# Performance work log

Hardware: AMD Instinct MI355X
Metric: run time of the kernel (lower is better)

The kernel has to match this reference:

```python
import jax, jax.numpy as jnp
import numpy as np

B, L = 4, 1024
V, D, H, NL = 32000, 256, 4, 8
S, DC, DI, NTYPES = 16, 4, 512, 5  # d_state, d_conv, d_inner=expand*d_model
NM, NA = 6, 2  # mamba blocks (layers 0,1,2,4,5,6), attention blocks (layers 3,7)


def layernorm(x, g, b):
    m = x.mean(-1, keepdims=True)
    v = x.var(-1, keepdims=True)
    return (x - m) / jnp.sqrt(v + 1e-5) * g + b


def mamba_block(x, g, b, in_w, conv_w, conv_b, xproj_w, dt_w, dt_b, A_log, Dp, out_w):
    res = x
    xn = layernorm(x, g, b)
    xz = xn @ in_w.T                          # [B,L,2*DI]
    xb, z = jnp.split(xz, 2, axis=-1)
    # depthwise causal conv1d (torch pads both sides then truncates to L == left-pad only)
    xc = jnp.transpose(xb, (0, 2, 1))         # [B,DI,L]
    xc = jax.lax.conv_general_dilated(xc, conv_w, (1,), [(DC - 1, 0)], feature_group_count=DI)
    xc = xc + conv_b[None, :, None]
    xb = jax.nn.silu(jnp.transpose(xc, (0, 2, 1)))  # [B,L,DI]
    A = -jnp.exp(A_log)                        # [DI,S]
    Bm, Cm = jnp.split(xb @ xproj_w.T, 2, axis=-1)  # each [B,L,S]
    dt = jax.nn.softplus(xb @ dt_w.T + dt_b)   # [B,L,DI]

    def step(h, inp):
        dt_t, B_t, C_t, x_t = inp              # [B,DI],[B,S],[B,S],[B,DI]
        A_bar = jnp.exp(dt_t[:, :, None] * A)  # [B,DI,S]
        h = A_bar * h + (dt_t * x_t)[:, :, None] * B_t[:, None, :]
        y = (h * C_t[:, None, :]).sum(-1) + Dp * x_t
        return h, y

    h0 = jnp.zeros((x.shape[0], DI, S), x.dtype)
    xs = (jnp.swapaxes(dt, 0, 1), jnp.swapaxes(Bm, 0, 1), jnp.swapaxes(Cm, 0, 1), jnp.swapaxes(xb, 0, 1))
    _, ys = jax.lax.scan(step, h0, xs)         # ys: [L,B,DI]
    y = jnp.swapaxes(ys, 0, 1) * jax.nn.silu(z)
    return y @ out_w.T + res


def attn_block(x, ts, mask, g, b, qkv_w, out_w, decay, ffg, ffb, ff1, ff2):
    Bs, Lq, Dm = x.shape
    dh = Dm // H
    res = x
    xn = layernorm(x, g, b)
    qkv = (xn @ qkv_w.T).reshape(Bs, Lq, 3, H, dh)
    q, k, v = qkv[:, :, 0], qkv[:, :, 1], qkv[:, :, 2]   # [B,L,H,dh]
    attn = jnp.einsum('bqhd,bkhd->bhqk', q, k) * dh ** -0.5
    t_diff = jnp.abs(ts[:, :, None] - ts[:, None, :])[:, None] / 24.0   # [B,1,L,L]
    attn = attn - jax.nn.softplus(decay)[None, :, None, None] * t_diff
    causal = jnp.triu(jnp.ones((Lq, Lq), bool), 1)
    attn = jnp.where(causal[None, None], -jnp.inf, attn)
    attn = jnp.where((mask == 0)[:, None, None, :], -jnp.inf, attn)
    attn = jax.nn.softmax(attn, axis=-1)       # dropout inactive (eval)
    out = jnp.einsum('bhqk,bkhd->bqhd', attn, v).reshape(Bs, Lq, Dm)
    x = res + out @ out_w.T
    xn2 = layernorm(x, ffg, ffb)
    return x + jax.nn.silu(xn2 @ ff1.T) @ ff2.T


def setup_inputs():
    key = jax.random.key(0)
    ks = iter(jax.random.split(key, 64))
    rn = lambda shape, s=0.02: jax.random.normal(next(ks), shape, jnp.float32) * s
    A_init = jnp.log(jnp.tile(jnp.arange(1, S + 1, dtype=jnp.float32)[None, None, :], (NM, DI, 1)))
    return dict(
        token_ids=jax.random.randint(next(ks), (B, L), 0, V, jnp.int32),
        token_types=jax.random.randint(next(ks), (B, L), 0, NTYPES, jnp.int32),
        timestamps=jax.random.uniform(next(ks), (B, L), jnp.float32) * 100.0,
        attention_mask=jnp.ones((B, L), jnp.int32),
        tok_emb=rn((V, D)).at[0].set(0.0),  # padding_idx=0
        type_emb=rn((NTYPES, D)),
        te_freq=rn((D // 2,), 0.01), te_phase=jnp.zeros((D // 2,)),
        te_w=rn((D, D)), te_b=jnp.zeros((D,)),
        m_norm_g=jnp.ones((NM, D)), m_norm_b=jnp.zeros((NM, D)),
        m_in_w=rn((NM, 2 * DI, D)),
        m_conv_w=rn((NM, DI, 1, DC)), m_conv_b=jnp.zeros((NM, DI)),
        m_xproj_w=rn((NM, 2 * S, DI)),
        m_dt_w=rn((NM, DI, DI)), m_dt_b=jnp.zeros((NM, DI)),
        m_Alog=A_init, m_D=jnp.ones((NM, DI)),
        m_out_w=rn((NM, D, DI)),
        a_norm_g=jnp.ones((NA, D)), a_norm_b=jnp.zeros((NA, D)),
        a_qkv_w=rn((NA, 3 * D, D)), a_out_w=rn((NA, D, D)),
        a_decay=jnp.full((NA, H), 0.01, jnp.float32),
        a_ffg=jnp.ones((NA, D)), a_ffb=jnp.zeros((NA, D)),
        a_ff1=rn((NA, 4 * D, D)), a_ff2=rn((NA, D, 4 * D)),
        f_g=jnp.ones((D,)), f_b=jnp.zeros((D,)),
        lm_w=rn((V, D)),
        re_w=rn((1, D)), re_b=jnp.zeros((1,)),
        mo_w=rn((1, D)), mo_b=jnp.zeros((1,)),
    )


def reference(token_ids, token_types, timestamps, attention_mask,
              tok_emb, type_emb, te_freq, te_phase, te_w, te_b,
              m_norm_g, m_norm_b, m_in_w, m_conv_w, m_conv_b, m_xproj_w,
              m_dt_w, m_dt_b, m_Alog, m_D, m_out_w,
              a_norm_g, a_norm_b, a_qkv_w, a_out_w, a_decay, a_ffg, a_ffb, a_ff1, a_ff2,
              f_g, f_b, lm_w, re_w, re_b, mo_w, mo_b):
    t = timestamps[..., None]
    freq = jax.nn.softplus(te_freq)
    enc = jnp.concatenate([jnp.sin(t * freq + te_phase), jnp.cos(t * freq + te_phase)], -1) @ te_w.T + te_b
    x = tok_emb[token_ids] + type_emb[token_types] + enc
    mi = ai = 0
    for i in range(NL):
        if (i + 1) % 4 == 0:
            x = attn_block(x, timestamps, attention_mask,
                           a_norm_g[ai], a_norm_b[ai], a_qkv_w[ai], a_out_w[ai], a_decay[ai],
                           a_ffg[ai], a_ffb[ai], a_ff1[ai], a_ff2[ai])
            ai += 1
        else:
            x = mamba_block(x, m_norm_g[mi], m_norm_b[mi], m_in_w[mi], m_conv_w[mi], m_conv_b[mi],
                            m_xproj_w[mi], m_dt_w[mi], m_dt_b[mi], m_Alog[mi], m_D[mi], m_out_w[mi])
            mi += 1
    x = layernorm(x, f_g, f_b)
    cls = x[:, 0, :]
    lm_logits = x @ lm_w.T
    readm = (cls @ re_w.T + re_b)[:, 0]
    mort = (cls @ mo_w.T + mo_b)[:, 0]
    return lm_logits, readm, mort
```

## Files before the change

### kernel.cpp

```cpp
#include <hip/hip_runtime.h>
#include <hip/hip_bf16.h>
#include <math.h>

#define BB 4
#define LL 1024
#define BL (BB*LL)
#define DD 256
#define VV 32000
#define HH 4
#define DH 64
#define SS 16
#define DCC 4
#define DII 512

typedef float f32x4 __attribute__((ext_vector_type(4)));
typedef short bh8  __attribute__((ext_vector_type(8)));
typedef unsigned short u16;

__device__ __forceinline__ float sp_f(float x) {
    return fmaxf(x, 0.f) + log1pf(expf(-fabsf(x)));
}
__device__ __forceinline__ float silu_f(float x) {
    return x / (1.f + expf(-x));
}
__device__ __forceinline__ short f2bf(float f) {
    __hip_bfloat16 h = __float2bfloat16(f);
    short s; __builtin_memcpy(&s, &h, 2); return s;
}
__device__ __forceinline__ float bf2f(u16 u) {
    unsigned v = ((unsigned)u) << 16;
    float f; __builtin_memcpy(&f, &v, 4); return f;
}

#define WB_TOT 5668864
#define LM_TOT 8192000
__global__ void cvtall_k(const float* __restrict__ te_w, const float* __restrict__ a_qkv,
                         const float* __restrict__ a_out, const float* __restrict__ a_ff1,
                         const float* __restrict__ a_ff2, const float* __restrict__ m_in,
                         const float* __restrict__ m_out, const float* __restrict__ m_dt,
                         const float* __restrict__ m_xp, const float* __restrict__ lm,
                         u16* __restrict__ dst, u16* __restrict__ dlm) {
    long i = ((long)blockIdx.x * 256 + threadIdx.x) * 4;
    const float* src; long off; u16* d; long doff;
    if (i >= WB_TOT) {
        long j = i - WB_TOT;
        if (j >= LM_TOT) return;
        src = lm; off = j; d = dlm; doff = j;
    } else {
        d = dst; doff = i;
        if      (i < 65536)   { src = te_w;  off = i; }
        else if (i < 458752)  { src = a_qkv; off = i - 65536; }
        else if (i < 589824)  { src = a_out; off = i - 458752; }
        else if (i < 1114112) { src = a_ff1; off = i - 589824; }
        else if (i < 1638400) { src = a_ff2; off = i - 1114112; }
        else if (i < 3211264) { src = m_in;  off = i - 1638400; }
        else if (i < 3997696) { src = m_out; off = i - 3211264; }
        else {
            long l = i - 3997696;
            int mi = (int)(l / 278528);
            long r = l - (long)mi * 278528;
            if (r < 262144) { src = m_dt + (long)mi * 262144; off = r; }
            else            { src = m_xp + (long)mi * 16384;  off = r - 262144; }
        }
    }
    float4 v = *(const float4*)(src + off);
    ushort4 u;
    u.x = (u16)f2bf(v.x); u.y = (u16)f2bf(v.y);
    u.z = (u16)f2bf(v.z); u.w = (u16)f2bf(v.w);
    *(ushort4*)(d + doff) = u;
}

__global__ void feat_k(const float* __restrict__ ts, const float* __restrict__ freq,
                       const float* __restrict__ phase, u16* __restrict__ feat) {
    int row = blockIdx.x, t = threadIdx.x;
    float tv = ts[row];
    int d = t & 127;
    float f = sp_f(freq[d]);
    float arg = tv * f + phase[d];
    feat[(size_t)row * DD + t] = (u16)f2bf((t < 128) ? sinf(arg) : cosf(arg));
}

__global__ void ln_k(const float* __restrict__ x, const float* __restrict__ g,
                     const float* __restrict__ bbias, u16* __restrict__ out) {
    __shared__ float red[8];
    int row = blockIdx.x, t = threadIdx.x;
    float v = x[(size_t)row * DD + t];
    float s = v;
    #pragma unroll
    for (int o = 32; o >= 1; o >>= 1) s += __shfl_xor(s, o);
    if ((t & 63) == 0) red[t >> 6] = s;
    __syncthreads();
    float mean = (red[0] + red[1] + red[2] + red[3]) * (1.f / 256.f);
    float d = v - mean;
    float s2 = d * d;
    #pragma unroll
    for (int o = 32; o >= 1; o >>= 1) s2 += __shfl_xor(s2, o);
    if ((t & 63) == 0) red[4 + (t >> 6)] = s2;
    __syncthreads();
    float var = (red[4] + red[5] + red[6] + red[7]) * (1.f / 256.f);
    out[(size_t)row * DD + t] = (u16)f2bf(d * rsqrtf(var + 1e-5f) * g[t] + bbias[t]);
}

template <int ACT, bool BOUT, bool VT>
__global__ __launch_bounds__(256) void lngemm_k(
    const float* __restrict__ X, const float* __restrict__ g, const float* __restrict__ bb,
    const u16* __restrict__ W, void* __restrict__ outv, u16* __restrict__ vt,
    int M, int N) {
    __shared__ __align__(16) char Abf[32768];
    __shared__ __align__(16) char Ws[8192];
    __shared__ float gs[256], bs[256];
    int tid = threadIdx.x;
    int bm = blockIdx.y * 64, bn = blockIdx.x * 64;
    gs[tid] = g[tid]; bs[tid] = bb[tid];

    int row = tid >> 2, part = tid & 3;
    const float* xr = X + (size_t)(bm + row) * 256 + part * 64;
    float4 vv[16];
    float s = 0.f, sq = 0.f;
    #pragma unroll
    for (int i = 0; i < 16; ++i) {
        vv[i] = *(const float4*)(xr + i * 4);
        s  += vv[i].x + vv[i].y + vv[i].z + vv[i].w;
        sq += vv[i].x * vv[i].x + vv[i].y * vv[i].y + vv[i].z * vv[i].z + vv[i].w * vv[i].w;
    }
    s += __shfl_xor(s, 1);  s += __shfl_xor(s, 2);
    sq += __shfl_xor(sq, 1); sq += __shfl_xor(sq, 2);
    float mean = s * (1.f / 256.f);
    float rstd = rsqrtf(sq * (1.f / 256.f) - mean * mean + 1e-5f);
    __syncthreads();
    #pragma unroll
    for (int i8 = 0; i8 < 8; ++i8) {
        bh8 p;
        #pragma unroll
        for (int j = 0; j < 8; ++j) {
            int e = i8 * 8 + j;
            float v = (j & 3) == 0 ? vv[e >> 2].x : (j & 3) == 1 ? vv[e >> 2].y
                    : (j & 3) == 2 ? vv[e >> 2].z : vv[e >> 2].w;
            int c = part * 64 + e;
            p[j] = f2bf((v - mean) * rstd * gs[c] + bs[c]);
        }
        *(bh8*)(Abf + (unsigned)((row * 512 + part * 128 + i8 * 16) ^ ((row & 7) << 4))) = p;
    }
    __syncthreads();

    int lane = tid & 63, wv = tid >> 6;
    int wm = wv >> 1, wn = wv & 1;
    int ro = lane & 15, kg = lane >> 4;
    f32x4 acc[2][2];
    #pragma unroll
    for (int i = 0; i < 2; ++i)
        #pragma unroll
        for (int j = 0; j < 2; ++j) acc[i][j] = (f32x4){0.f, 0.f, 0.f, 0.f};

    const u16* gw = W + (size_t)(bn + row) * 256 + part * 16;
    bool wvalid = (bn + row) < N;
    unsigned swb = (unsigned)(row * 128 + part * 32);
    unsigned sx  = (unsigned)((row & 7) << 4);
    for (int kk = 0; kk < 256; kk += 64) {
        if (kk) __syncthreads();
        bh8 w0 = {}, w1 = {};
        if (wvalid) { w0 = *(const bh8*)(gw + kk); w1 = *(const bh8*)(gw + kk + 8); }
        *(bh8*)(Ws + (swb ^ sx)) = w0;
        *(bh8*)(Ws + ((swb + 16) ^ sx)) = w1;
        __syncthreads();
        #pragma unroll
        for (int ks = 0; ks < 2; ++ks) {
            bh8 af[2], bf_[2];
            #pragma unroll
            for (int m = 0; m < 2; ++m) {
                int r = wm * 32 + m * 16 + ro;
                af[m] = *(const bh8*)(Abf + (unsigned)((r * 512 + kk * 2 + ks * 64 + kg * 16) ^ ((r & 7) << 4)));
            }
            #pragma unroll
            for (int n = 0; n < 2; ++n) {
                int r = wn * 32 + n * 16 + ro;
                bf_[n] = *(const bh8*)(Ws + (unsigned)((r * 128 + ks * 64 + kg * 16) ^ ((r & 7) << 4)));
            }
            #pragma unroll
            for (int m = 0; m < 2; ++m)
                #pragma unroll
                for (int n = 0; n < 2; ++n)
                    acc[m][n] = __builtin_amdgcn_mfma_f32_16x16x32_bf16(af[m], bf_[n], acc[m][n], 0, 0, 0);
        }
    }

    float* outf = (float*)outv;
    u16*   outb = (u16*)outv;
    int cr = (lane >> 4) * 4, cc = lane & 15;
    #pragma unroll
    for (int mf = 0; mf < 2; ++mf) {
        #pragma unroll
        for (int nf = 0; nf < 2; ++nf) {
            int n = bn + wn * 32 + nf * 16 + cc;
            if (n >= N) continue;
            int mbase = bm + wm * 32 + mf * 16 + cr;
            f32x4 a = acc[mf][nf];
            #pragma unroll
            for (int r = 0; r < 4; ++r) {
                float v = a[r];
                if (ACT == 1) v = silu_f(v);
                if (BOUT) outb[(size_t)(mbase + r) * N + n] = (u16)f2bf(v);
                else      outf[(size_t)(mbase + r) * N + n] = v;
            }
            if (VT && n >= 512) {
                int hh = (n - 512) >> 6, dd = (n - 512) & 63;
                int b_ = mbase >> 10, l = mbase & 1023;
                ushort4 uv;
                uv.x = (u16)f2bf(acc[mf][nf][0]); uv.y = (u16)f2bf(acc[mf][nf][1]);
                uv.z = (u16)f2bf(acc[mf][nf][2]); uv.w = (u16)f2bf(acc[mf][nf][3]);
                *(ushort4*)(vt + ((((size_t)b_ * HH + hh) * DH + dd) << 10) + l) = uv;
            }
        }
    }
}

template <int ACT, bool HASB, bool HASR, bool BOUT>
__global__ __launch_bounds__(256) void bgemm_k(
    const u16* __restrict__ A, const u16* __restrict__ W,
    const float* __restrict__ bias, const float* __restrict__ res,
    void* __restrict__ outv, float* __restrict__ out2, int M, int N, int K,
    const int* __restrict__ ids, const int* __restrict__ typ,
    const float* __restrict__ tok, const float* __restrict__ tpe) {
    __shared__ __align__(16) char lds[16384];
    char* As = lds;
    char* Ws = lds + 8192;
    int tid = threadIdx.x;
    int bm = blockIdx.y * 64, bn = blockIdx.x * 64;
    int row = tid >> 2, q = tid & 3;
    int lane = tid & 63, wv = tid >> 6;
    int wm = wv >> 1, wn = wv & 1;
    int ro = lane & 15, kg = lane >> 4;

    f32x4 acc[2][2];
    #pragma unroll
    for (int i = 0; i < 2; ++i)
        #pragma unroll
        for (int j = 0; j < 2; ++j) acc[i][j] = (f32x4){0.f, 0.f, 0.f, 0.f};

    const u16* ga = A + (size_t)(bm + row) * K + q * 16;
    const u16* gw = W + (size_t)(bn + row) * K + q * 16;
    bool wvalid = (bn + row) < N;
    unsigned swb = (unsigned)(row * 128 + q * 32);
    unsigned sx  = (unsigned)((row & 7) << 4);

    for (int kk = 0; kk < K; kk += 64) {
        if (kk) __syncthreads();
        {
            *(bh8*)(As + (swb ^ sx)) = *(const bh8*)(ga);
            *(bh8*)(As + ((swb + 16) ^ sx)) = *(const bh8*)(ga + 8);
            bh8 w0 = {}, w1 = {};
            if (wvalid) { w0 = *(const bh8*)(gw); w1 = *(const bh8*)(gw + 8); }
            *(bh8*)(Ws + (swb ^ sx)) = w0;
            *(bh8*)(Ws + ((swb + 16) ^ sx)) = w1;
        }
        ga += 64; gw += 64;
        __syncthreads();
        #pragma unroll
        for (int ks = 0; ks < 2; ++ks) {
            bh8 af[2], bf_[2];
            #pragma unroll
            for (int m = 0; m < 2; ++m) {
                int r = wm * 32 + m * 16 + ro;
                af[m] = *(const bh8*)(As + (unsigned)((r * 128 + ks * 64 + kg * 16) ^ ((r & 7) << 4)));
            }
            #pragma unroll
            for (int n = 0; n < 2; ++n) {
                int r = wn * 32 + n * 16 + ro;
                bf_[n] = *(const bh8*)(Ws + (unsigned)((r * 128 + ks * 64 + kg * 16) ^ ((r & 7) << 4)));
            }
            #pragma unroll
            for (int m = 0; m < 2; ++m)
                #pragma unroll
                for (int n = 0; n < 2; ++n)
                    acc[m][n] = __builtin_amdgcn_mfma_f32_16x16x32_bf16(af[m], bf_[n], acc[m][n], 0, 0, 0);
        }
    }

    float* outf = (float*)outv;
    u16*   outb = (u16*)outv;
    int cr = (lane >> 4) * 4, cc = lane & 15;
    #pragma unroll
    for (int mf = 0; mf < 2; ++mf) {
        #pragma unroll
        for (int nf = 0; nf < 2; ++nf) {
            int n = bn + wn * 32 + nf * 16 + cc;
            if (n >= N) continue;
            int mbase = bm + wm * 32 + mf * 16 + cr;
            f32x4 a = acc[mf][nf];
            #pragma unroll
            for (int r = 0; r < 4; ++r) {
                float v = a[r];
                int m = mbase + r;
                if (ACT == 3) {
                    if (n < 512) outf[(size_t)m * 512 + n] = sp_f(v + bias[n]);
                    else         out2[(size_t)m * 32 + (n - 512)] = v;
                } else if (ACT == 4) {
                    v += bias[n] + tok[(size_t)ids[m] * DD + n] + tpe[(size_t)typ[m] * DD + n];
                    outf[(size_t)m * N + n] = v;
                } else {
                    if (HASB) v += bias[n];
                    if (ACT == 1) v = silu_f(v);
                    if (HASR) v += res[(size_t)m * N + n];
                    if (BOUT) outb[(size_t)m * N + n] = (u16)f2bf(v);
                    else      outf[(size_t)m * N + n] = v;
                }
            }
        }
    }
}

__global__ __launch_bounds__(256) void mgemmL_k(
    const u16* __restrict__ A, const u16* __restrict__ W,
    float* __restrict__ out, int M, int N, int K) {
    __shared__ __align__(16) char lds[32768];
    char* As = lds;
    char* Ws = lds + 16384;
    int lid = blockIdx.y * 32 + blockIdx.x;
    int xcd = lid & 7, wk = lid >> 3;
    int nt = xcd * 32 + (wk >> 5);
    int mt = wk & 31;
    if (nt * 128 >= N) return;
    int bm = mt * 128, bn = nt * 128;

    int tid = threadIdx.x;
    int row = tid >> 1, half = tid & 1;
    int lane = tid & 63, wv = tid >> 6;
    int wm = wv >> 1, wn = wv & 1;
    int ro = lane & 15, kg = lane >> 4;

    f32x4 acc[4][4];
    #pragma unroll
    for (int i = 0; i < 4; ++i)
        #pragma unroll
        for (int j = 0; j < 4; ++j) acc[i][j] = (f32x4){0.f, 0.f, 0.f, 0.f};

    const u16* ga = A + (size_t)(bm + row) * K + half * 32;
    const u16* gw = W + (size_t)(bn + row) * K + half * 32;
    unsigned swb = (unsigned)(row * 128 + half * 64);
    unsigned sx  = (unsigned)((row & 7) << 4);

    for (int kk = 0; kk < K; kk += 64) {
        if (kk) __syncthreads();
        #pragma unroll
        for (int j = 0; j < 4; ++j) {
            *(bh8*)(As + ((swb + j * 16) ^ sx)) = *(const bh8*)(ga + j * 8);
            *(bh8*)(Ws + ((swb + j * 16) ^ sx)) = *(const bh8*)(gw + j * 8);
        }
        ga += 64; gw += 64;
        __syncthreads();
        #pragma unroll
        for (int ks = 0; ks < 2; ++ks) {
            bh8 af[4], bf_[4];
            #pragma unroll
            for (int m = 0; m < 4; ++m) {
                int r = wm * 64 + m * 16 + ro;
                af[m] = *(const bh8*)(As + (unsigned)((r * 128 + ks * 64 + kg * 16) ^ ((r & 7) << 4)));
            }
            #pragma unroll
            for (int n = 0; n < 4; ++n) {
                int r = wn * 64 + n * 16 + ro;
                bf_[n] = *(const bh8*)(Ws + (unsigned)((r * 128 + ks * 64 + kg * 16) ^ ((r & 7) << 4)));
            }
            #pragma unroll
            for (int m = 0; m < 4; ++m)
                #pragma unroll
                for (int n = 0; n < 4; ++n)
                    acc[m][n] = __builtin_amdgcn_mfma_f32_16x16x32_bf16(af[m], bf_[n], acc[m][n], 0, 0, 0);
        }
    }

    int cr = (lane >> 4) * 4, cc = lane & 15;
    #pragma unroll
    for (int mf = 0; mf < 4; ++mf) {
        #pragma unroll
        for (int nf = 0; nf < 4; ++nf) {
            int n = bn + wn * 64 + nf * 16 + cc;
            int mbase = bm + wm * 64 + mf * 16 + cr;
            f32x4 a = acc[mf][nf];
            #pragma unroll
            for (int r = 0; r < 4; ++r)
                out[(size_t)(mbase + r) * N + n] = a[r];
        }
    }
}

__global__ void conv_k(const u16* __restrict__ xz, const float* __restrict__ w,
                       const float* __restrict__ cb, u16* __restrict__ xbb) {
    int idx = blockIdx.x * blockDim.x + threadIdx.x;
    int c = idx & (DII - 1);
    int row = idx >> 9;
    int l = row & (LL - 1);
    int base = row - l;
    const float* wc = w + c * DCC;
    float s = cb[c];
    #pragma unroll
    for (int j = 0; j < DCC; ++j) {
        int ll = l - (DCC - 1) + j;
        if (ll >= 0) s = fmaf(wc[j], bf2f(xz[((size_t)(base + ll)) * (2 * DII) + c]), s);
    }
    xbb[(size_t)idx] = (u16)f2bf(silu_f(s));
}

__global__ __launch_bounds__(256) void scanA_k(
    const float* __restrict__ dt, const u16* __restrict__ xb,
    const float* __restrict__ bc, const float* __restrict__ Alog,
    float* __restrict__ P, float* __restrict__ Lc, int nc, int cln) {
    int bid = blockIdx.x;
    int per_b = nc * 2;
    int b = bid / per_b;
    int rem = bid - b * per_b;
    int c = rem >> 1;
    int di = (rem & 1) * 256 + threadIdx.x;
    float A[SS], ap[SS], h[SS];
    #pragma unroll
    for (int s = 0; s < SS; ++s) { A[s] = -expf(Alog[di * SS + s]); ap[s] = 1.f; h[s] = 0.f; }
    for (int l = c * cln; l < c * cln + cln; ++l) {
        size_t base = (size_t)b * LL + l;
        float dtv = dt[base * DII + di];
        float xv  = bf2f(xb[base * DII + di]);
        const float* Bt = bc + base * (2 * SS);
        float u = dtv * xv;
        #pragma unroll
        for (int s = 0; s < SS; ++s) {
            float a = expf(dtv * A[s]);
            ap[s] *= a;
            h[s] = fmaf(a, h[s], u * Bt[s]);
        }
    }
    size_t o = (((size_t)c * BB + b) * DII + di) * SS;
    #pragma unroll
    for (int j = 0; j < 4; ++j) {
        *(f32x4*)(P  + o + j * 4) = (f32x4){ap[j*4], ap[j*4+1], ap[j*4+2], ap[j*4+3]};
        *(f32x4*)(Lc + o + j * 4) = (f32x4){h[j*4],  h[j*4+1],  h[j*4+2],  h[j*4+3]};
    }
}

__global__ __launch_bounds__(256) void scanC_k(
    const float* __restrict__ dt, const u16* __restrict__ xb,
    const float* __restrict__ bc, const u16* __restrict__ xz,
    const float* __restrict__ Alog, const float* __restrict__ Dp,
    const float* __restrict__ P, const float* __restrict__ Lc,
    u16* __restrict__ y, int nc, int cln) {
    int bid = blockIdx.x;
    int per_b = nc * 2;
    int b = bid / per_b;
    int rem = bid - b * per_b;
    int c = rem >> 1;
    int di = (rem & 1) * 256 + threadIdx.x;
    float A[SS];
    #pragma unroll
    for (int s = 0; s < SS; ++s) A[s] = -expf(Alog[di * SS + s]);
    f32x4 h4[4];
    #pragma unroll
    for (int j = 0; j < 4; ++j) h4[j] = (f32x4){0.f, 0.f, 0.f, 0.f};
    for (int cc = 0; cc < c; ++cc) {
        size_t o = (((size_t)cc * BB + b) * DII + di) * SS;
        #pragma unroll
        for (int j = 0; j < 4; ++j) {
            f32x4 p  = *(const f32x4*)(P  + o + j * 4);
            f32x4 lc = *(const f32x4*)(Lc + o + j * 4);
            h4[j] = p * h4[j] + lc;
        }
    }
    float h[SS];
    #pragma unroll
    for (int j = 0; j < 4; ++j) {
        h[j*4+0] = h4[j][0]; h[j*4+1] = h4[j][1]; h[j*4+2] = h4[j][2]; h[j*4+3] = h4[j][3];
    }
    float Dv = Dp[di];
    for (int l = c * cln; l < c * cln + cln; ++l) {
        size_t base = (size_t)b * LL + l;
        float dtv = dt[base * DII + di];
        float xv  = bf2f(xb[base * DII + di]);
        float zv  = bf2f(xz[base * (2 * DII) + DII + di]);
        const float* Bt = bc + base * (2 * SS);
        float u = dtv * xv;
        float acc = 0.f;
        #pragma unroll
        for (int s = 0; s < SS; ++s) {
            float a = expf(dtv * A[s]);
            h[s] = fmaf(a, h[s], u * Bt[s]);
            acc = fmaf(h[s], Bt[SS + s], acc);
        }
        y[base * DII + di] = (u16)f2bf(fmaf(Dv, xv, acc) * silu_f(zv));
    }
}

__global__ __launch_bounds__(256) void fattn_k(
    const u16* __restrict__ qkv, const u16* __restrict__ vt,
    const float* __restrict__ ts, const int* __restrict__ mask,
    const float* __restrict__ decay, u16* __restrict__ out) {
    __shared__ __align__(16) char ksm[8192];
    __shared__ __align__(16) char vsm[8192];
    __shared__ __align__(16) char psm[8192];
    __shared__ float tsk[64];
    __shared__ int   msk[64];

    int tid = threadIdx.x;
    int lane = tid & 63, wvi = tid >> 6;
    int qt = blockIdx.x & 15;
    int h  = (blockIdx.x >> 4) & 3;
    int b  = blockIdx.x >> 6;
    int q0 = qt * 64;
    int g = lane >> 4, c = lane & 15;

    bh8 qf[2];
    {
        const u16* qrow = qkv + ((size_t)(b * LL + q0 + wvi * 16 + c)) * (3 * DD) + h * DH;
        qf[0] = *(const bh8*)(qrow + g * 8);
        qf[1] = *(const bh8*)(qrow + 32 + g * 8);
    }
    float tq[4];
    #pragma unroll
    for (int j = 0; j < 4; ++j) tq[j] = ts[b * LL + q0 + wvi * 16 + g * 4 + j];
    float spd = sp_f(decay[h]);

    f32x4 o[4];
    #pragma unroll
    for (int n = 0; n < 4; ++n) o[n] = (f32x4){0.f, 0.f, 0.f, 0.f};
    float mrow[4] = {-INFINITY, -INFINITY, -INFINITY, -INFINITY};
    float drow[4] = {0.f, 0.f, 0.f, 0.f};

    char* pw = psm + wvi * 2048;

    for (int kt = 0; kt <= qt; ++kt) {
        int k0 = kt * 64;
        __syncthreads();
        {
            int row = tid >> 2, qq = tid & 3;
            unsigned sw = (unsigned)((row & 7) << 4);
            unsigned base = (unsigned)(row * 128 + qq * 32);
            const u16* kr = qkv + ((size_t)(b * LL + k0 + row)) * (3 * DD) + DD + h * DH + qq * 16;
            *(bh8*)(ksm + (base ^ sw)) = *(const bh8*)(kr);
            *(bh8*)(ksm + ((base + 16) ^ sw)) = *(const bh8*)(kr + 8);
            const u16* vr = vt + ((((size_t)b * HH + h) * DH + row) << 10) + k0 + qq * 16;
            *(bh8*)(vsm + (base ^ sw)) = *(const bh8*)(vr);
            *(bh8*)(vsm + ((base + 16) ^ sw)) = *(const bh8*)(vr + 8);
            if (tid < 64) { tsk[tid] = ts[b * LL + k0 + tid]; msk[tid] = mask[b * LL + k0 + tid]; }
        }
        __syncthreads();

        f32x4 sf[4];
        #pragma unroll
        for (int n = 0; n < 4; ++n) sf[n] = (f32x4){0.f, 0.f, 0.f, 0.f};
        #pragma unroll
        for (int ks = 0; ks < 2; ++ks) {
            #pragma unroll
            for (int nf = 0; nf < 4; ++nf) {
                int rr = nf * 16 + c;
                bh8 kf = *(const bh8*)(ksm + (unsigned)((rr * 128 + ks * 64 + g * 16) ^ ((rr & 7) << 4)));
                sf[nf] = __builtin_amdgcn_mfma_f32_16x16x32_bf16(qf[ks], kf, sf[nf], 0, 0, 0);
            }
        }
        float mnew[4] = {mrow[0], mrow[1], mrow[2], mrow[3]};
        #pragma unroll
        for (int nf = 0; nf < 4; ++nf) {
            int kk = c + 16 * nf;
            float tk = tsk[kk];
            bool md = (msk[kk] == 0);
            #pragma unroll
            for (int j = 0; j < 4; ++j) {
                int qrow = q0 + wvi * 16 + g * 4 + j;
                float s = sf[nf][j] * 0.125f - spd * fabsf(tq[j] - tk) * (1.f / 24.f);
                bool dead = md || (k0 + kk > qrow);
                s = dead ? -INFINITY : s;
                sf[nf][j] = s;
                mnew[j] = fmaxf(mnew[j], s);
            }
        }
        #pragma unroll
        for (int off = 1; off <= 8; off <<= 1)
            #pragma unroll
            for (int j = 0; j < 4; ++j) mnew[j] = fmaxf(mnew[j], __shfl_xor(mnew[j], off));
        float scl[4], psum[4];
        #pragma unroll
        for (int j = 0; j < 4; ++j) {
            scl[j] = (mnew[j] == -INFINITY) ? 1.f : expf(mrow[j] - mnew[j]);
            psum[j] = 0.f;
            mrow[j] = mnew[j];
        }
        #pragma unroll
        for (int nf = 0; nf < 4; ++nf) {
            #pragma unroll
            for (int j = 0; j < 4; ++j) {
                float s = sf[nf][j];
                float p = (s == -INFINITY) ? 0.f : expf(s - mrow[j]);
                psum[j] += p;
                int row = g * 4 + j;
                *(short*)(pw + (unsigned)((row * 128 + (c + 16 * nf) * 2) ^ ((row & 7) << 4))) = f2bf(p);
            }
        }
        #pragma unroll
        for (int off = 1; off <= 8; off <<= 1)
            #pragma unroll
            for (int j = 0; j < 4; ++j) psum[j] += __shfl_xor(psum[j], off);
        #pragma unroll
        for (int j = 0; j < 4; ++j) drow[j] = drow[j] * scl[j] + psum[j];
        #pragma unroll
        for (int n = 0; n < 4; ++n)
            #pragma unroll
            for (int j = 0; j < 4; ++j) o[n][j] *= scl[j];
        #pragma unroll
        for (int ks = 0; ks < 2; ++ks) {
            bh8 pf = *(const bh8*)(pw + (unsigned)((c * 128 + ks * 64 + g * 16) ^ ((c & 7) << 4)));
            #pragma unroll
            for (int n = 0; n < 4; ++n) {
                int rr = n * 16 + c;
                bh8 vf = *(const bh8*)(vsm + (unsigned)((rr * 128 + ks * 64 + g * 16) ^ ((rr & 7) << 4)));
                o[n] = __builtin_amdgcn_mfma_f32_16x16x32_bf16(pf, vf, o[n], 0, 0, 0);
            }
        }
    }
    #pragma unroll
    for (int n = 0; n < 4; ++n) {
        #pragma unroll
        for (int j = 0; j < 4; ++j) {
            int qrow = q0 + wvi * 16 + g * 4 + j;
            out[((size_t)(b * LL + qrow)) * DD + h * DH + c + 16 * n] = (u16)f2bf(o[n][j] / drow[j]);
        }
    }
}

__global__ __launch_bounds__(64) void heads_k(
    const u16* __restrict__ xn, const float* __restrict__ re_w, const float* __restrict__ re_b,
    const float* __restrict__ mo_w, const float* __restrict__ mo_b, float* __restrict__ out) {
    int lane = threadIdx.x;
    int b = blockIdx.x & 3;
    int which = blockIdx.x >> 2;
    const float* wv = which ? mo_w : re_w;
    const u16* row = xn + (size_t)b * LL * DD;
    float s = 0.f;
    #pragma unroll
    for (int d = 0; d < DD / 64; ++d) s = fmaf(bf2f(row[lane + d * 64]), wv[lane + d * 64], s);
    #pragma unroll
    for (int o = 32; o >= 1; o >>= 1) s += __shfl_xor(s, o);
    if (lane == 0) out[(size_t)VV * BL + which * 4 + b] = s + (which ? mo_b[0] : re_b[0]);
}

extern "C" void kernel_launch(void* const* d_in, const int* in_sizes, int n_in,
                              void* d_out, int out_size, void* d_ws, size_t ws_size,
                              hipStream_t stream) {
    const int*   ids      = (const int*)  d_in[0];
    const int*   typ      = (const int*)  d_in[1];
    const float* ts       = (const float*)d_in[2];
    const int*   amask    = (const int*)  d_in[3];
    const float* tok_emb  = (const float*)d_in[4];
    const float* type_emb = (const float*)d_in[5];
    const float* te_freq  = (const float*)d_in[6];
    const float* te_phase = (const float*)d_in[7];
    const float* te_w     = (const float*)d_in[8];
    const float* te_b     = (const float*)d_in[9];
    const float* m_norm_g = (const float*)d_in[10];
    const float* m_norm_b = (const float*)d_in[11];
    const float* m_in_w   = (const float*)d_in[12];
    const float* m_conv_w = (const float*)d_in[13];
    const float* m_conv_b = (const float*)d_in[14];
    const float* m_xproj  = (const float*)d_in[15];
    const float* m_dt_w   = (const float*)d_in[16];
    const float* m_dt_b   = (const float*)d_in[17];
    const float* m_Alog   = (const float*)d_in[18];
    const float* m_D      = (const float*)d_in[19];
    const float* m_out_w  = (const float*)d_in[20];
    const float* a_norm_g = (const float*)d_in[21];
    const float* a_norm_b = (const float*)d_in[22];
    const float* a_qkv_w  = (const float*)d_in[23];
    const float* a_out_w  = (const float*)d_in[24];
    const float* a_decay  = (const float*)d_in[25];
    const float* a_ffg    = (const float*)d_in[26];
    const float* a_ffb    = (const float*)d_in[27];
    const float* a_ff1    = (const float*)d_in[28];
    const float* a_ff2    = (const float*)d_in[29];
    const float* f_g      = (const float*)d_in[30];
    const float* f_b      = (const float*)d_in[31];
    const float* lm_w     = (const float*)d_in[32];
    const float* re_w     = (const float*)d_in[33];
    const float* re_b     = (const float*)d_in[34];
    const float* mo_w     = (const float*)d_in[35];
    const float* mo_b     = (const float*)d_in[36];

    float* out = (float*)d_out;
    float* ws  = (float*)d_ws;

    float* x    = ws;
    u16*   xnb  = (u16*)(ws + 1048576);
    u16*   t1   = (u16*)(ws + 1572864);
    u16*   b1   = (u16*)(ws + 3670016);
    u16*   b2   = (u16*)(ws + 5767168);
    float* t3   = ws + 6815744;
    float* t5   = ws + 8912896;
    u16*   vtb  = (u16*)(ws + 9043968);
    u16*   wbuf = (u16*)(ws + 9568256);
    u16*   wlm  = (u16*)(ws + 12402688);
    float* sP   = ws + 16498688;
    int nc = (ws_size >= (size_t)(16498688 + 2 * 64 * 32768) * 4) ? 64 : 32;
    float* sL = sP + (size_t)nc * 32768;
    int cln = LL / nc;

    const u16* w_te  = wbuf;
    const u16* w_qkv = wbuf + 65536;
    const u16* w_ao  = wbuf + 458752;
    const u16* w_ff1 = wbuf + 589824;
    const u16* w_ff2 = wbuf + 1114112;
    const u16* w_min = wbuf + 1638400;
    const u16* w_mo  = wbuf + 3211264;
    const u16* w_dtx = wbuf + 3997696;

    cvtall_k<<<(WB_TOT + LM_TOT) / 1024, 256, 0, stream>>>(
        te_w, a_qkv_w, a_out_w, a_ff1, a_ff2, m_in_w, m_out_w, m_dt_w, m_xproj, lm_w, wbuf, wlm);
    feat_k<<<BL, 256, 0, stream>>>(ts, te_freq, te_phase, b1);
    bgemm_k<4, true, false, false><<<dim3(4, BL / 64), 256, 0, stream>>>(
        b1, w_te, te_b, nullptr, x, nullptr, BL, DD, DD, ids, typ, tok_emb, type_emb);

    int mi = 0, ai = 0;
    for (int i = 0; i < 8; ++i) {
        if ((i + 1) % 4 == 0) {
            lngemm_k<0, true, true><<<dim3(12, BL / 64), 256, 0, stream>>>(
                x, a_norm_g + ai * DD, a_norm_b + ai * DD,
                w_qkv + (size_t)ai * 196608, t1, vtb, BL, 3 * DD);
            fattn_k<<<BB * HH * (LL / 64), 256, 0, stream>>>(
                t1, vtb, ts, amask, a_decay + ai * HH, b1);
            bgemm_k<0, false, true, false><<<dim3(4, BL / 64), 256, 0, stream>>>(
                b1, w_ao + (size_t)ai * 65536, nullptr, x, x, nullptr, BL, DD, DD,
                nullptr, nullptr, nullptr, nullptr);
            lngemm_k<1, true, false><<<dim3(16, BL / 64), 256, 0, stream>>>(
                x, a_ffg + ai * DD, a_ffb + ai * DD,
                w_ff1 + (size_t)ai * 262144, b1, nullptr, BL, 4 * DD);
            bgemm_k<0, false, true, false><<<dim3(4, BL / 64), 256, 0, stream>>>(
                b1, w_ff2 + (size_t)ai * 262144, nullptr, x, x, nullptr, BL, DD, 4 * DD,
                nullptr, nullptr, nullptr, nullptr);
            ++ai;
        } else {
            lngemm_k<0, true, false><<<dim3(16, BL / 64), 256, 0, stream>>>(
                x, m_norm_g + mi * DD, m_norm_b + mi * DD,
                w_min + (size_t)mi * 262144, t1, nullptr, BL, 2 * DII);
            conv_k<<<(BL * DII) / 256, 256, 0, stream>>>(
                t1, m_conv_w + (size_t)mi * DII * DCC, m_conv_b + mi * DII, b1);
            bgemm_k<3, true, false, false><<<dim3(9, BL / 64), 256, 0, stream>>>(
                b1, w_dtx + (size_t)mi * 278528, m_dt_b + mi * DII, nullptr, t3, t5, BL, 544, DII,
                nullptr, nullptr, nullptr, nullptr);
            scanA_k<<<BB * nc * 2, 256, 0, stream>>>(
                t3, b1, t5, m_Alog + (size_t)mi * DII * SS, sP, sL, nc, cln);
            scanC_k<<<BB * nc * 2, 256, 0, stream>>>(
                t3, b1, t5, t1, m_Alog + (size_t)mi * DII * SS, m_D + mi * DII, sP, sL, b2, nc, cln);
            bgemm_k<0, false, true, false><<<dim3(4, BL / 64), 256, 0, stream>>>(
                b2, w_mo + (size_t)mi * 131072, nullptr, x, x, nullptr, BL, DD, DII,
                nullptr, nullptr, nullptr, nullptr);
            ++mi;
        }
    }

    ln_k<<<BL, 256, 0, stream>>>(x, f_g, f_b, xnb);
    mgemmL_k<<<dim3(32, 256), 256, 0, stream>>>(xnb, wlm, out, BL, VV, DD);
    heads_k<<<8, 64, 0, stream>>>(xnb, re_w, re_b, mo_w, mo_b, out);
}
```

Before: 1.414 ms.

## Replace two-pass chunked scan with per-channel block scan; split-K narrow GEMMs

The Mamba selective scan moves from a two-kernel chunked scheme (chunk summaries in global memory, then a serial prefix over chunks) to a single kernel. Each block handles one (batch, channel) pair and runs a Hillis-Steele parallel scan in LDS over 256 threads, each covering 4 timesteps. Separately, the N=256 residual GEMMs get a split-K variant with 512 threads: two K-halves are computed and reduced through shared memory, raising parallelism for the small grids. The trade-offs are strided global loads of dt/xb per channel (poor coalescing), repeated exp work, and log-step synchronisation with heavy LDS traffic across 16 states.

```diff
diff --git a/kernel.cpp b/kernel.cpp
--- a/kernel.cpp
+++ b/kernel.cpp
@@ -218,9 +218,7 @@
 __global__ __launch_bounds__(256) void bgemm_k(
     const u16* __restrict__ A, const u16* __restrict__ W,
     const float* __restrict__ bias, const float* __restrict__ res,
-    void* __restrict__ outv, float* __restrict__ out2, int M, int N, int K,
-    const int* __restrict__ ids, const int* __restrict__ typ,
-    const float* __restrict__ tok, const float* __restrict__ tpe) {
+    void* __restrict__ outv, float* __restrict__ out2, int M, int N, int K) {
     __shared__ __align__(16) char lds[16384];
     char* As = lds;
     char* Ws = lds + 8192;
@@ -294,15 +292,110 @@
                 if (ACT == 3) {
                     if (n < 512) outf[(size_t)m * 512 + n] = sp_f(v + bias[n]);
                     else         out2[(size_t)m * 32 + (n - 512)] = v;
-                } else if (ACT == 4) {
-                    v += bias[n] + tok[(size_t)ids[m] * DD + n] + tpe[(size_t)typ[m] * DD + n];
-                    outf[(size_t)m * N + n] = v;
                 } else {
                     if (HASB) v += bias[n];
                     if (ACT == 1) v = silu_f(v);
                     if (HASR) v += res[(size_t)m * N + n];
                     if (BOUT) outb[(size_t)m * N + n] = (u16)f2bf(v);
                     else      outf[(size_t)m * N + n] = v;
+                }
+            }
+        }
+    }
+}
+
+template <int ACT, bool HASB, bool HASR>
+__global__ __launch_bounds__(512) void bgemmsk_k(
+    const u16* __restrict__ A, const u16* __restrict__ W,
+    const float* __restrict__ bias, const float* __restrict__ res,
+    float* __restrict__ out, int M, int N, int K,
+    const int* __restrict__ ids, const int* __restrict__ typ,
+    const float* __restrict__ tok, const float* __restrict__ tpe) {
+    __shared__ __align__(16) char As[2][8192];
+    __shared__ __align__(16) char Ws[2][8192];
+    __shared__ float red[4][32][33];
+    int tid = threadIdx.x;
+    int kh = tid >> 8;
+    int t  = tid & 255;
+    int bm = blockIdx.y * 64, bn = blockIdx.x * 64;
+    int row = t >> 2, q = t & 3;
+    int lane = tid & 63;
+    int wq = (tid >> 6) & 3;
+    int wm = wq >> 1, wn = wq & 1;
+    int ro = lane & 15, kg = lane >> 4;
+
+    f32x4 acc[2][2];
+    #pragma unroll
+    for (int i = 0; i < 2; ++i)
+        #pragma unroll
+        for (int j = 0; j < 2; ++j) acc[i][j] = (f32x4){0.f, 0.f, 0.f, 0.f};
+
+    int khalf = K >> 1;
+    const u16* ga = A + (size_t)(bm + row) * K + kh * khalf + q * 16;
+    const u16* gw = W + (size_t)(bn + row) * K + kh * khalf + q * 16;
+    unsigned swb = (unsigned)(row * 128 + q * 32);
+    unsigned sx  = (unsigned)((row & 7) << 4);
+
+    for (int kk = 0; kk < khalf; kk += 64) {
+        if (kk) __syncthreads();
+        *(bh8*)(As[kh] + (swb ^ sx)) = *(const bh8*)(ga);
+        *(bh8*)(As[kh] + ((swb + 16) ^ sx)) = *(const bh8*)(ga + 8);
+        *(bh8*)(Ws[kh] + (swb ^ sx)) = *(const bh8*)(gw);
+        *(bh8*)(Ws[kh] + ((swb + 16) ^ sx)) = *(const bh8*)(gw + 8);
+        ga += 64; gw += 64;
+        __syncthreads();
+        #pragma unroll
+        for (int ks = 0; ks < 2; ++ks) {
+            bh8 af[2], bf_[2];
+            #pragma unroll
+            for (int m = 0; m < 2; ++m) {
+                int r = wm * 32 + m * 16 + ro;
+                af[m] = *(const bh8*)(As[kh] + (unsigned)((r * 128 + ks * 64 + kg * 16) ^ ((r & 7) << 4)));
+            }
+            #pragma unroll
+            for (int n = 0; n < 2; ++n) {
+                int r = wn * 32 + n * 16 + ro;
+                bf_[n] = *(const bh8*)(Ws[kh] + (unsigned)((r * 128 + ks * 64 + kg * 16) ^ ((r & 7) << 4)));
+            }
+            #pragma unroll
+            for (int m = 0; m < 2; ++m)
+                #pragma unroll
+                for (int n = 0; n < 2; ++n)
+                    acc[m][n] = __builtin_amdgcn_mfma_f32_16x16x32_bf16(af[m], bf_[n], acc[m][n], 0, 0, 0);
+        }
+    }
+
+    int cr = (lane >> 4) * 4, cc = lane & 15;
+    __syncthreads();
+    if (kh == 1) {
+        #pragma unroll
+        for (int mf = 0; mf < 2; ++mf)
+            #pragma unroll
+            for (int nf = 0; nf < 2; ++nf)
+                #pragma unroll
+                for (int r = 0; r < 4; ++r)
+                    red[wq][mf * 16 + cr + r][nf * 16 + cc] = acc[mf][nf][r];
+    }
+    __syncthreads();
+    if (kh == 0) {
+        #pragma unroll
+        for (int mf = 0; mf < 2; ++mf) {
+            #pragma unroll
+            for (int nf = 0; nf < 2; ++nf) {
+                int n = bn + wn * 32 + nf * 16 + cc;
+                if (n >= N) continue;
+                int mbase = bm + wm * 32 + mf * 16 + cr;
+                #pragma unroll
+                for (int r = 0; r < 4; ++r) {
+                    float v = acc[mf][nf][r] + red[wq][mf * 16 + cr + r][nf * 16 + cc];
+                    int m = mbase + r;
+                    if (ACT == 4) {
+                        v += bias[n] + tok[(size_t)ids[m] * DD + n] + tpe[(size_t)typ[m] * DD + n];
+                    } else {
+                        if (HASB) v += bias[n];
+                        if (HASR) v += res[(size_t)m * N + n];
+                    }
+                    out[(size_t)m * N + n] = v;
                 }
             }
         }
@@ -401,88 +494,90 @@
     xbb[(size_t)idx] = (u16)f2bf(silu_f(s));
 }
 
-__global__ __launch_bounds__(256) void scanA_k(
-    const float* __restrict__ dt, const u16* __restrict__ xb,
-    const float* __restrict__ bc, const float* __restrict__ Alog,
-    float* __restrict__ P, float* __restrict__ Lc, int nc, int cln) {
-    int bid = blockIdx.x;
-    int per_b = nc * 2;
-    int b = bid / per_b;
-    int rem = bid - b * per_b;
-    int c = rem >> 1;
-    int di = (rem & 1) * 256 + threadIdx.x;
-    float A[SS], ap[SS], h[SS];
-    #pragma unroll
-    for (int s = 0; s < SS; ++s) { A[s] = -expf(Alog[di * SS + s]); ap[s] = 1.f; h[s] = 0.f; }
-    for (int l = c * cln; l < c * cln + cln; ++l) {
-        size_t base = (size_t)b * LL + l;
-        float dtv = dt[base * DII + di];
-        float xv  = bf2f(xb[base * DII + di]);
-        const float* Bt = bc + base * (2 * SS);
-        float u = dtv * xv;
+__global__ __launch_bounds__(256) void scan_k(
+    const float* __restrict__ dt,
+    const u16* __restrict__ xb,
+    const float* __restrict__ bc,
+    const u16* __restrict__ xz,
+    const float* __restrict__ Alog, const float* __restrict__ Dp,
+    u16* __restrict__ y) {
+    __shared__ float pa[SS][257];
+    __shared__ float ph[SS][257];
+    int di = blockIdx.x & (DII - 1);
+    int b  = blockIdx.x >> 9;
+    int t  = threadIdx.x;
+    int l0 = t * 4;
+    size_t rb = (size_t)(b * LL + l0);
+
+    float A[SS];
+    #pragma unroll
+    for (int s = 0; s < SS; ++s) A[s] = -expf(Alog[di * SS + s]);
+
+    float dtv[4], xv[4];
+    #pragma unroll
+    for (int j = 0; j < 4; ++j) {
+        dtv[j] = dt[(rb + j) * DII + di];
+        xv[j]  = bf2f(xb[(rb + j) * DII + di]);
+    }
+
+    float Pa[SS], Ph[SS];
+    #pragma unroll
+    for (int j = 0; j < 4; ++j) {
+        float u = dtv[j] * xv[j];
+        const float* bt = bc + (rb + j) * (2 * SS);
         #pragma unroll
         for (int s = 0; s < SS; ++s) {
-            float a = expf(dtv * A[s]);
-            ap[s] *= a;
-            h[s] = fmaf(a, h[s], u * Bt[s]);
-        }
-    }
-    size_t o = (((size_t)c * BB + b) * DII + di) * SS;
+            float a = expf(dtv[j] * A[s]);
+            float w = u * bt[s];
+            if (j == 0) { Pa[s] = a; Ph[s] = w; }
+            else        { Pa[s] *= a; Ph[s] = fmaf(a, Ph[s], w); }
+        }
+    }
+    #pragma unroll
+    for (int s = 0; s < SS; ++s) { pa[s][t] = Pa[s]; ph[s][t] = Ph[s]; }
+    __syncthreads();
+
+    #pragma unroll
+    for (int off = 1; off < 256; off <<= 1) {
+        float qa[SS], qh[SS];
+        bool has = (t >= off);
+        if (has) {
+            #pragma unroll
+            for (int s = 0; s < SS; ++s) { qa[s] = pa[s][t - off]; qh[s] = ph[s][t - off]; }
+        }
+        __syncthreads();
+        if (has) {
+            #pragma unroll
+            for (int s = 0; s < SS; ++s) {
+                ph[s][t] = fmaf(pa[s][t], qh[s], ph[s][t]);
+                pa[s][t] *= qa[s];
+            }
+        }
+        __syncthreads();
+    }
+
+    float h[SS];
+    if (t == 0) {
+        #pragma unroll
+        for (int s = 0; s < SS; ++s) h[s] = 0.f;
+    } else {
+        #pragma unroll
+        for (int s = 0; s < SS; ++s) h[s] = ph[s][t - 1];
+    }
+    float Dv = Dp[di];
     #pragma unroll
     for (int j = 0; j < 4; ++j) {
-        *(f32x4*)(P  + o + j * 4) = (f32x4){ap[j*4], ap[j*4+1], ap[j*4+2], ap[j*4+3]};
-        *(f32x4*)(Lc + o + j * 4) = (f32x4){h[j*4],  h[j*4+1],  h[j*4+2],  h[j*4+3]};
-    }
-}
-
-__global__ __launch_bounds__(256) void scanC_k(
-    const float* __restrict__ dt, const u16* __restrict__ xb,
-    const float* __restrict__ bc, const u16* __restrict__ xz,
-    const float* __restrict__ Alog, const float* __restrict__ Dp,
-    const float* __restrict__ P, const float* __restrict__ Lc,
-    u16* __restrict__ y, int nc, int cln) {
-    int bid = blockIdx.x;
-    int per_b = nc * 2;
-    int b = bid / per_b;
-    int rem = bid - b * per_b;
-    int c = rem >> 1;
-    int di = (rem & 1) * 256 + threadIdx.x;
-    float A[SS];
-    #pragma unroll
-    for (int s = 0; s < SS; ++s) A[s] = -expf(Alog[di * SS + s]);
-    f32x4 h4[4];
-    #pragma unroll
-    for (int j = 0; j < 4; ++j) h4[j] = (f32x4){0.f, 0.f, 0.f, 0.f};
-    for (int cc = 0; cc < c; ++cc) {
-        size_t o = (((size_t)cc * BB + b) * DII + di) * SS;
-        #pragma unroll
-        for (int j = 0; j < 4; ++j) {
-            f32x4 p  = *(const f32x4*)(P  + o + j * 4);
-            f32x4 lc = *(const f32x4*)(Lc + o + j * 4);
-            h4[j] = p * h4[j] + lc;
-        }
-    }
-    float h[SS];
-    #pragma unroll
-    for (int j = 0; j < 4; ++j) {
-        h[j*4+0] = h4[j][0]; h[j*4+1] = h4[j][1]; h[j*4+2] = h4[j][2]; h[j*4+3] = h4[j][3];
-    }
-    float Dv = Dp[di];
-    for (int l = c * cln; l < c * cln + cln; ++l) {
-        size_t base = (size_t)b * LL + l;
-        float dtv = dt[base * DII + di];
-        float xv  = bf2f(xb[base * DII + di]);
-        float zv  = bf2f(xz[base * (2 * DII) + DII + di]);
-        const float* Bt = bc + base * (2 * SS);
-        float u = dtv * xv;
+        float u = dtv[j] * xv[j];
+        const float* bt = bc + (rb + j) * (2 * SS);
         float acc = 0.f;
         #pragma unroll
         for (int s = 0; s < SS; ++s) {
-            float a = expf(dtv * A[s]);
-            h[s] = fmaf(a, h[s], u * Bt[s]);
-            acc = fmaf(h[s], Bt[SS + s], acc);
-        }
-        y[base * DII + di] = (u16)f2bf(fmaf(Dv, xv, acc) * silu_f(zv));
+            float a = expf(dtv[j] * A[s]);
+            h[s] = fmaf(a, h[s], u * bt[s]);
+            acc = fmaf(h[s], bt[SS + s], acc);
+        }
+        float zv = bf2f(xz[(rb + j) * (2 * DII) + DII + di]);
+        y[(rb + j) * DII + di] = (u16)f2bf(fmaf(Dv, xv[j], acc) * silu_f(zv));
     }
 }
 
@@ -691,10 +786,6 @@
     u16*   vtb  = (u16*)(ws + 9043968);
     u16*   wbuf = (u16*)(ws + 9568256);
     u16*   wlm  = (u16*)(ws + 12402688);
-    float* sP   = ws + 16498688;
-    int nc = (ws_size >= (size_t)(16498688 + 2 * 64 * 32768) * 4) ? 64 : 32;
-    float* sL = sP + (size_t)nc * 32768;
-    int cln = LL / nc;
 
     const u16* w_te  = wbuf;
     const u16* w_qkv = wbuf + 65536;
@@ -708,8 +799,8 @@
     cvtall_k<<<(WB_TOT + LM_TOT) / 1024, 256, 0, stream>>>(
         te_w, a_qkv_w, a_out_w, a_ff1, a_ff2, m_in_w, m_out_w, m_dt_w, m_xproj, lm_w, wbuf, wlm);
     feat_k<<<BL, 256, 0, stream>>>(ts, te_freq, te_phase, b1);
-    bgemm_k<4, true, false, false><<<dim3(4, BL / 64), 256, 0, stream>>>(
-        b1, w_te, te_b, nullptr, x, nullptr, BL, DD, DD, ids, typ, tok_emb, type_emb);
+    bgemmsk_k<4, true, false><<<dim3(4, BL / 64), 512, 0, stream>>>(
+        b1, w_te, te_b, nullptr, x, BL, DD, DD, ids, typ, tok_emb, type_emb);
 
     int mi = 0, ai = 0;
     for (int i = 0; i < 8; ++i) {
@@ -719,14 +810,14 @@
                 w_qkv + (size_t)ai * 196608, t1, vtb, BL, 3 * DD);
             fattn_k<<<BB * HH * (LL / 64), 256, 0, stream>>>(
                 t1, vtb, ts, amask, a_decay + ai * HH, b1);
-            bgemm_k<0, false, true, false><<<dim3(4, BL / 64), 256, 0, stream>>>(
-                b1, w_ao + (size_t)ai * 65536, nullptr, x, x, nullptr, BL, DD, DD,
+            bgemmsk_k<0, false, true><<<dim3(4, BL / 64), 512, 0, stream>>>(
+                b1, w_ao + (size_t)ai * 65536, nullptr, x, x, BL, DD, DD,
                 nullptr, nullptr, nullptr, nullptr);
             lngemm_k<1, true, false><<<dim3(16, BL / 64), 256, 0, stream>>>(
                 x, a_ffg + ai * DD, a_ffb + ai * DD,
                 w_ff1 + (size_t)ai * 262144, b1, nullptr, BL, 4 * DD);
-            bgemm_k<0, false, true, false><<<dim3(4, BL / 64), 256, 0, stream>>>(
-                b1, w_ff2 + (size_t)ai * 262144, nullptr, x, x, nullptr, BL, DD, 4 * DD,
+            bgemmsk_k<0, false, true><<<dim3(4, BL / 64), 512, 0, stream>>>(
+                b1, w_ff2 + (size_t)ai * 262144, nullptr, x, x, BL, DD, 4 * DD,
                 nullptr, nullptr, nullptr, nullptr);
             ++ai;
         } else {
@@ -736,14 +827,11 @@
             conv_k<<<(BL * DII) / 256, 256, 0, stream>>>(
                 t1, m_conv_w + (size_t)mi * DII * DCC, m_conv_b + mi * DII, b1);
             bgemm_k<3, true, false, false><<<dim3(9, BL / 64), 256, 0, stream>>>(
-                b1, w_dtx + (size_t)mi * 278528, m_dt_b + mi * DII, nullptr, t3, t5, BL, 544, DII,
-                nullptr, nullptr, nullptr, nullptr);
-            scanA_k<<<BB * nc * 2, 256, 0, stream>>>(
-                t3, b1, t5, m_Alog + (size_t)mi * DII * SS, sP, sL, nc, cln);
-            scanC_k<<<BB * nc * 2, 256, 0, stream>>>(
-                t3, b1, t5, t1, m_Alog + (size_t)mi * DII * SS, m_D + mi * DII, sP, sL, b2, nc, cln);
-            bgemm_k<0, false, true, false><<<dim3(4, BL / 64), 256, 0, stream>>>(
-                b2, w_mo + (size_t)mi * 131072, nullptr, x, x, nullptr, BL, DD, DII,
+                b1, w_dtx + (size_t)mi * 278528, m_dt_b + mi * DII, nullptr, t3, t5, BL, 544, DII);
+            scan_k<<<BB * DII, 256, 0, stream>>>(
+                t3, b1, t5, t1, m_Alog + (size_t)mi * DII * SS, m_D + mi * DII, b2);
+            bgemmsk_k<0, false, true><<<dim3(4, BL / 64), 512, 0, stream>>>(
+                b2, w_mo + (size_t)mi * 131072, nullptr, x, x, BL, DD, DII,
                 nullptr, nullptr, nullptr, nullptr);
             ++mi;
         }
```

Result: slower. 1.446 ms (+2.3%).
